# Kernel optimization log

Hardware: AMD Instinct MI355X
Metric: run time of the kernel (lower is better)

Reference implementation:

```python
import jax, jax.numpy as jnp
import numpy as np

N = 6000          # RPN proposals pre-NMS
C = 64            # ROI feature channels
NUM_CLASSES = 21  # VOC-style classes
THR = 0.7         # NMS IoU threshold (generate_rois default)


def setup_inputs() -> dict:
    key = jax.random.key(0)
    k = jax.random.split(key, 8)
    # valid boxes: x1<x2, y1<y2 inside a 1000x1000 image
    xy = jax.random.uniform(k[0], (N, 2)) * 900.0
    wh = jax.random.uniform(k[1], (N, 2)) * 90.0 + 10.0
    boxes = jnp.concatenate([xy, xy + wh], axis=-1)
    scores = jax.random.uniform(k[2], (N,))
    roi_features = jax.random.normal(k[3], (N, 14, 14, C))
    W1 = jax.random.normal(k[4], (2 * 2 * C, 1024)) * 0.02
    b1 = jnp.zeros((1024,))
    Wc = jax.random.normal(k[5], (1024, NUM_CLASSES)) * 0.02
    bc = jnp.zeros((NUM_CLASSES,))
    Wr = jax.random.normal(k[6], (1024, 4)) * 0.02
    br = jnp.zeros((4,))
    return dict(boxes=boxes, scores=scores, roi_features=roi_features,
                W1=W1, b1=b1, Wc=Wc, bc=bc, Wr=Wr, br=br)


def _nms_keep(boxes, scores, thr):
    # Greedy sequential NMS, identical math to the Python loop:
    # highest score kept, suppress any remaining box with IoU >= thr.
    order = jnp.argsort(-scores)
    b = boxes[order]
    x1, y1, x2, y2 = b[:, 0], b[:, 1], b[:, 2], b[:, 3]
    area = (x2 - x1) * (y2 - y1)
    ix1 = jnp.maximum(x1[:, None], x1[None, :])
    iy1 = jnp.maximum(y1[:, None], y1[None, :])
    ix2 = jnp.minimum(x2[:, None], x2[None, :])
    iy2 = jnp.minimum(y2[:, None], y2[None, :])
    inter = jnp.maximum(0.0, ix2 - ix1) * jnp.maximum(0.0, iy2 - iy1)  # [N,N]
    iou = inter / (area[:, None] + area[None, :] - inter)
    n = b.shape[0]
    idx = jnp.arange(n)

    def body(i, keep):
        # if box i survived, suppress later boxes with IoU >= thr
        sup = (iou[i] >= thr) & (idx > i) & keep[i]
        return keep & ~sup

    keep_sorted = jax.lax.fori_loop(0, n, body, jnp.ones(n, dtype=bool))
    return jnp.zeros(n, dtype=bool).at[order].set(keep_sorted)


def reference(boxes, scores, roi_features, W1, b1, Wc, bc, Wr, br):
    keep = _nms_keep(boxes, scores, THR)  # [N] bool, NMS-selected ROIs
    n = roi_features.shape[0]
    # MaxPooling2D(pool_size=7, stride=7): 14x14 -> 2x2
    pooled = roi_features.reshape(n, 2, 7, 2, 7, C).max(axis=(2, 4))
    flat = pooled.reshape(n, -1)                      # [N, 256]
    h = jax.nn.relu(flat @ W1 + b1)                   # [N, 1024]
    cls = jax.nn.softmax(h @ Wc + bc, axis=-1)        # [N, num_classes]
    reg = h @ Wr + br                                 # [N, 4]
    kf = keep.astype(cls.dtype)[:, None]
    # suppressed ROIs zeroed (static-shape stand-in for the variable-length selection)
    return cls * kf, reg * kf, keep
```

## Files before the change

kernel.cpp:

```cpp
#include <hip/hip_runtime.h>

using u64 = unsigned long long;
using u32 = unsigned int;
using u16 = unsigned short;

typedef short bf16x8 __attribute__((ext_vector_type(8)));
typedef float f32x4  __attribute__((ext_vector_type(4)));

#define NB   6000
#define CB94 94
#define THRF 0.7f

__device__ __forceinline__ u16 f2bf(float f) {
    u32 u = __float_as_uint(f);
    return (u16)((u + 0x7FFFu + ((u >> 16) & 1u)) >> 16);
}

__device__ __forceinline__ void gload_lds16(const void* g, void* l) {
    __builtin_amdgcn_global_load_lds((const __attribute__((address_space(1))) void*)g,
                                     (__attribute__((address_space(3))) void*)l, 16, 0, 0);
}


__global__ void rank_kernel(const float* __restrict__ scores, int* __restrict__ rank) {
    __shared__ float sj[256];
    int t = threadIdx.x;
    int j0 = blockIdx.y * 256;
    int jj = j0 + t;
    sj[t] = (jj < NB) ? scores[jj] : 0.f;
    __syncthreads();
    int i = blockIdx.x * 256 + t;
    if (i >= NB) return;
    float si = scores[i];
    int jn = min(256, NB - j0);
    int cnt = 0;
    for (int k = 0; k < jn; ++k) {
        float s = sj[k];
        int j = j0 + k;
        cnt += (s > si) || (s == si && j < i);
    }
    if (cnt) atomicAdd(&rank[i], cnt);
}

__global__ void scatter_kernel(const float* __restrict__ boxes, const int* __restrict__ rank,
                               int* __restrict__ order, float4* __restrict__ sboxes) {
    int i = blockIdx.x * 256 + threadIdx.x;
    if (i >= NB) return;
    int r = rank[i];
    order[r] = i;
    sboxes[r] = ((const float4*)boxes)[i];
}

__global__ __launch_bounds__(64) void mask_kernel(const float4* __restrict__ sboxes,
                                                  u64* __restrict__ mask,
                                                  u64* __restrict__ bitmap) {
    int cb = blockIdx.x, rb = blockIdx.y;
    if (cb < rb) return;
    __shared__ float4 cbox[64];
    __shared__ float  carea[64];
    int t = threadIdx.x;
    int j = cb * 64 + t;
    if (j < NB) {
        float4 b = sboxes[j];
        cbox[t] = b;
        carea[t] = (b.z - b.x) * (b.w - b.y);
    }
    __syncthreads();
    int i = rb * 64 + t;
    if (i >= NB) return;
    float4 a = sboxes[i];
    float aarea = (a.z - a.x) * (a.w - a.y);
    int jn = min(64, NB - cb * 64);
    u64 bits = 0;
    for (int k = 0; k < jn; ++k) {
        int jg = cb * 64 + k;
        if (jg <= i) continue;
        float4 b = cbox[k];
        float iw = fmaxf(fminf(a.z, b.z) - fmaxf(a.x, b.x), 0.f);
        float ih = fmaxf(fminf(a.w, b.w) - fmaxf(a.y, b.y), 0.f);
        float inter = __fmul_rn(iw, ih);
        float denom = __fsub_rn(__fadd_rn(aarea, carea[k]), inter);
        float iou = __fdiv_rn(inter, denom);
        if (iou >= THRF) bits |= 1ull << k;
    }
    mask[(size_t)i * CB94 + cb] = bits;
    if (bits) atomicOr(&bitmap[i * 2 + (cb >> 6)], 1ull << (cb & 63));
}

__global__ __launch_bounds__(256) void scan_kernel(const u64* __restrict__ gmask,
                                                   const u64* __restrict__ gbitmap,
                                                   const int* __restrict__ order,
                                                   float* __restrict__ keepF,
                                                   float* __restrict__ out) {
    __shared__ u64 diagLDS[CB94 * 64];
    __shared__ u64 bmLDS[NB * 2];
    __shared__ u64 removedLDS[CB94];
    int t = threadIdx.x;
    for (int idx = t; idx < CB94 * 64; idx += 256) {
        int w = idx >> 6, b = idx & 63;
        int r = w * 64 + b;
        diagLDS[idx] = (r < NB) ? gmask[(size_t)r * CB94 + w] : 0ull;
    }
    for (int idx = t; idx < NB * 2; idx += 256) bmLDS[idx] = gbitmap[idx];
    for (int idx = t; idx < CB94; idx += 256) removedLDS[idx] = 0ull;
    __syncthreads();

    if (t < 64) {
        int l = t;
        for (int w = 0; w < CB94; ++w) {
            u64 rm = removedLDS[w];
            u64 dg = diagLDS[w * 64 + l];
            u64 valid = (w == CB94 - 1) ? ((1ull << 48) - 1ull) : ~0ull;
            u64 nz = __ballot(dg != 0ull);
            u64 cand = nz & ~rm & valid;
            while (cand) {
                int b = __ffsll(cand) - 1;
                u64 db = __shfl(dg, b, 64);
                rm |= db;
                cand &= ~rm;
                cand &= ~(1ull << b);
            }
            if (l == 0) removedLDS[w] = rm;
            u64 kept = valid & ~rm;
            if ((kept >> l) & 1ull) {
                int r = w * 64 + l;
                u64 bm0 = bmLDS[2 * r], bm1 = bmLDS[2 * r + 1];
                if (w < 63) bm0 &= ~((2ull << w) - 1ull); else bm0 = 0ull;
                if (w >= 64) bm1 &= ~((2ull << (w - 64)) - 1ull);
                while (bm0) {
                    int tt = __ffsll(bm0) - 1;
                    bm0 &= bm0 - 1;
                    u64 mw = gmask[(size_t)r * CB94 + tt];
                    atomicOr(&removedLDS[tt], mw);
                }
                while (bm1) {
                    int b2 = __ffsll(bm1) - 1;
                    bm1 &= bm1 - 1;
                    int tt = 64 + b2;
                    u64 mw = gmask[(size_t)r * CB94 + tt];
                    atomicOr(&removedLDS[tt], mw);
                }
            }
        }
    }
    __syncthreads();
    for (int k = t; k < NB; k += 256) {
        int sup = (int)((removedLDS[k >> 6] >> (k & 63)) & 1ull);
        float kf = sup ? 0.f : 1.f;
        int orig = order[k];
        keepF[orig] = kf;
        out[150000 + orig] = kf;
    }
}


__global__ __launch_bounds__(256) void pool_kernel(const float* __restrict__ roi,
                                                   u16* __restrict__ flat) {
    int t = threadIdx.x;
    int n = blockIdx.x * 4 + (t >> 6);
    int lane = t & 63;
    int p = lane >> 4, li = lane & 15;
    int ph = p >> 1, pw = p & 1;
    const float4* base = (const float4*)roi;
    float mx0 = -3.4e38f, mx1 = -3.4e38f, mx2 = -3.4e38f, mx3 = -3.4e38f;
#pragma unroll
    for (int i = 0; i < 7; ++i)
#pragma unroll
        for (int j = 0; j < 7; ++j) {
            float4 v = base[((n * 14 + ph * 7 + i) * 14 + pw * 7 + j) * 16 + li];
            mx0 = fmaxf(mx0, v.x); mx1 = fmaxf(mx1, v.y);
            mx2 = fmaxf(mx2, v.z); mx3 = fmaxf(mx3, v.w);
        }
    int ob = n * 256 + p * 64 + li * 4;
    u64 pack = (u64)f2bf(mx0) | ((u64)f2bf(mx1) << 16) | ((u64)f2bf(mx2) << 32) | ((u64)f2bf(mx3) << 48);
    *(u64*)&flat[ob] = pack;
}

__global__ void prep_w1t(const float* __restrict__ W1, u16* __restrict__ w1t) {
    int idx = blockIdx.x * 256 + threadIdx.x;
    if (idx >= 1024 * 256) return;
    int n = idx >> 8, k = idx & 255;
    w1t[idx] = f2bf(W1[k * 1024 + n]);
}

__global__ void prep_w2t(const float* __restrict__ Wc, const float* __restrict__ Wr,
                         u16* __restrict__ w2t) {
    int idx = blockIdx.x * 256 + threadIdx.x;
    if (idx >= 32 * 1024) return;
    int o = idx >> 10, k = idx & 1023;
    float v = 0.f;
    if (o < 21) v = Wc[k * 21 + o];
    else if (o < 25) v = Wr[k * 4 + (o - 21)];
    w2t[idx] = f2bf(v);
}

__global__ __launch_bounds__(256) void gemm1_kernel(const u16* __restrict__ flat,
                                                    const u16* __restrict__ w1t,
                                                    const float* __restrict__ b1,
                                                    u16* __restrict__ h) {
    __shared__ __align__(16) u16 Alds[128 * 32];
    __shared__ __align__(16) u16 Blds[128 * 32];
    int t = threadIdx.x;
    int c0 = blockIdx.x * 128;
    int r0 = blockIdx.y * 128;
    int lane = t & 63, wid = t >> 6, wr = wid >> 1, wc = wid & 1;
    int lrow = lane & 15, kblk = lane >> 4;
    f32x4 acc[4][4] = {};
    for (int step = 0; step < 8; ++step) {
        int k0 = step * 32;
#pragma unroll
        for (int it = 0; it < 2; ++it) {
            int chunk = it * 256 + t;
            int row = chunk >> 2, kc = chunk & 3;
            int ar = r0 + row; ar = ar < (NB - 1) ? ar : (NB - 1);
            gload_lds16(flat + ar * 256 + k0 + kc * 8, &Alds[chunk * 8]);
            gload_lds16(w1t + (c0 + row) * 256 + k0 + kc * 8, &Blds[chunk * 8]);
        }
        __syncthreads();
        bf16x8 a[4], b[4];
#pragma unroll
        for (int m = 0; m < 4; ++m) a[m] = *(const bf16x8*)&Alds[(wr * 64 + m * 16 + lrow) * 32 + kblk * 8];
#pragma unroll
        for (int n = 0; n < 4; ++n) b[n] = *(const bf16x8*)&Blds[(wc * 64 + n * 16 + lrow) * 32 + kblk * 8];
#pragma unroll
        for (int m = 0; m < 4; ++m)
#pragma unroll
            for (int n = 0; n < 4; ++n)
                acc[m][n] = __builtin_amdgcn_mfma_f32_16x16x32_bf16(a[m], b[n], acc[m][n], 0, 0, 0);
        __syncthreads();
    }
    int rj = lane >> 4;
#pragma unroll
    for (int n = 0; n < 4; ++n) {
        int col = c0 + wc * 64 + n * 16 + lrow;
        float bias = b1[col];
#pragma unroll
        for (int m = 0; m < 4; ++m) {
            int rbase = r0 + wr * 64 + m * 16 + rj * 4;
#pragma unroll
            for (int j = 0; j < 4; ++j) {
                int r = rbase + j;
                if (r < NB) {
                    float v = acc[m][n][j] + bias;
                    v = v > 0.f ? v : 0.f;
                    h[r * 1024 + col] = f2bf(v);
                }
            }
        }
    }
}

__global__ __launch_bounds__(256) void gemm2_kernel(const u16* __restrict__ h,
                                                    const u16* __restrict__ w2t,
                                                    float* __restrict__ scores) {
    __shared__ __align__(16) u16 Alds[4 * 64 * 32];
    __shared__ __align__(16) u16 Blds[4 * 32 * 32];
    int t = threadIdx.x, lane = t & 63, w = t >> 6;
    int r0 = blockIdx.x * 64;
    int lrow = lane & 15, kblk = lane >> 4;
    f32x4 acc[2] = {};
    for (int round = 0; round < 8; ++round) {
        int kr0 = round * 128;
#pragma unroll
        for (int it = 0; it < 4; ++it) {
            int chunk = it * 256 + t;
            int kk = chunk >> 8, rem = chunk & 255, row = rem >> 2, kc = rem & 3;
            int ar = r0 + row; ar = ar < (NB - 1) ? ar : (NB - 1);
            gload_lds16(h + ar * 1024 + kr0 + kk * 32 + kc * 8, &Alds[chunk * 8]);
        }
#pragma unroll
        for (int it = 0; it < 2; ++it) {
            int chunk = it * 256 + t;
            int kk = chunk >> 7, rem = chunk & 127, orow = rem >> 2, kc = rem & 3;
            gload_lds16(w2t + orow * 1024 + kr0 + kk * 32 + kc * 8, &Blds[chunk * 8]);
        }
        __syncthreads();
#pragma unroll
        for (int kk = 0; kk < 4; ++kk) {
            bf16x8 a = *(const bf16x8*)&Alds[kk * 2048 + (w * 16 + lrow) * 32 + kblk * 8];
#pragma unroll
            for (int nf = 0; nf < 2; ++nf) {
                bf16x8 b = *(const bf16x8*)&Blds[kk * 1024 + (nf * 16 + lrow) * 32 + kblk * 8];
                acc[nf] = __builtin_amdgcn_mfma_f32_16x16x32_bf16(a, b, acc[nf], 0, 0, 0);
            }
        }
        __syncthreads();
    }
#pragma unroll
    for (int nf = 0; nf < 2; ++nf) {
        int col = nf * 16 + lrow;
#pragma unroll
        for (int j = 0; j < 4; ++j) {
            int r = r0 + w * 16 + (lane >> 4) * 4 + j;
            if (r < NB) scores[r * 32 + col] = acc[nf][j];
        }
    }
}

__global__ void epilogue_kernel(const float* __restrict__ scores, const float* __restrict__ keepF,
                                const float* __restrict__ bc, const float* __restrict__ br,
                                float* __restrict__ out) {
    int r = blockIdx.x * 256 + threadIdx.x;
    if (r >= NB) return;
    float kf = keepF[r];
    float lg[21];
    float m = -3.4e38f;
#pragma unroll
    for (int o = 0; o < 21; ++o) {
        lg[o] = scores[r * 32 + o] + bc[o];
        m = fmaxf(m, lg[o]);
    }
    float s = 0.f;
#pragma unroll
    for (int o = 0; o < 21; ++o) {
        lg[o] = expf(lg[o] - m);
        s += lg[o];
    }
    float inv = kf / s;
#pragma unroll
    for (int o = 0; o < 21; ++o) out[r * 21 + o] = lg[o] * inv;
#pragma unroll
    for (int o = 0; o < 4; ++o) out[126000 + r * 4 + o] = (scores[r * 32 + 21 + o] + br[o]) * kf;
}


extern "C" void kernel_launch(void* const* d_in, const int* in_sizes, int n_in,
                              void* d_out, int out_size, void* d_ws, size_t ws_size,
                              hipStream_t stream) {
    (void)in_sizes; (void)n_in; (void)out_size; (void)ws_size;
    const float* boxes  = (const float*)d_in[0];
    const float* scores = (const float*)d_in[1];
    const float* roi    = (const float*)d_in[2];
    const float* W1     = (const float*)d_in[3];
    const float* b1     = (const float*)d_in[4];
    const float* Wc     = (const float*)d_in[5];
    const float* bc     = (const float*)d_in[6];
    const float* Wr     = (const float*)d_in[7];
    const float* br     = (const float*)d_in[8];
    float* out = (float*)d_out;

    char* ws = (char*)d_ws;
    const size_t O_RANK   = 0;
    const size_t O_ORDER  = 24064;
    const size_t O_SBOX   = 48128;
    const size_t O_BITMAP = 144128;
    const size_t O_MASK   = 240128;
    const size_t O_KEEPF  = 4752128;
    const size_t O_FLAT   = 4776128;
    const size_t O_W1T    = 7848128;
    const size_t O_W2T    = 8372416;
    const size_t O_H      = 8437952;
    const size_t O_SCORES = 20725952;

    int*    rank   = (int*)(ws + O_RANK);
    int*    order  = (int*)(ws + O_ORDER);
    float4* sboxes = (float4*)(ws + O_SBOX);
    u64*    bitmap = (u64*)(ws + O_BITMAP);
    u64*    mask   = (u64*)(ws + O_MASK);
    float*  keepF  = (float*)(ws + O_KEEPF);
    u16*    flat   = (u16*)(ws + O_FLAT);
    u16*    w1t    = (u16*)(ws + O_W1T);
    u16*    w2t    = (u16*)(ws + O_W2T);
    u16*    h      = (u16*)(ws + O_H);
    float*  sc2    = (float*)(ws + O_SCORES);

    hipMemsetAsync(ws + O_RANK, 0, 24000, stream);
    hipMemsetAsync(ws + O_BITMAP, 0, 96000, stream);

    pool_kernel<<<1500, 256, 0, stream>>>(roi, flat);
    prep_w1t<<<1024, 256, 0, stream>>>(W1, w1t);
    prep_w2t<<<128, 256, 0, stream>>>(Wc, Wr, w2t);

    rank_kernel<<<dim3(24, 24), 256, 0, stream>>>(scores, rank);
    scatter_kernel<<<24, 256, 0, stream>>>(boxes, rank, order, sboxes);
    mask_kernel<<<dim3(CB94, CB94), 64, 0, stream>>>(sboxes, mask, bitmap);

    gemm1_kernel<<<dim3(8, 47), 256, 0, stream>>>(flat, w1t, b1, h);

    scan_kernel<<<1, 256, 0, stream>>>(mask, bitmap, order, keepF, out);

    gemm2_kernel<<<CB94, 256, 0, stream>>>(h, w2t, sc2);
    epilogue_kernel<<<24, 256, 0, stream>>>(sc2, keepF, bc, br, out);
}
```

Baseline: 220.9 us.

## Fuse front-end kernels, rank+scatter, contiguous diag mask, and gemm2 with epilogue

Merges pooling, weight transposes, and the score ranking with scatter into one heterogeneous front kernel. Rank is now computed per 64-row block without atomics, and the bitmap is cleared in place, which removes both memsets. The mask kernel now uses 256-thread blocks and also writes a contiguous diagonal array, so the single-block scan loads it with coalesced reads instead of strided ones. gemm2 is fused with the softmax/regression epilogue through LDS, removing a scores round-trip and a launch. The cost is a serial 6000-score loop per rank block, about 94 blocks, and some block-size imbalance within the fused front kernel.

```diff
diff --git a/kernel.cpp b/kernel.cpp
--- a/kernel.cpp
+++ b/kernel.cpp
@@ -22,51 +22,105 @@
 }
 
 
-__global__ void rank_kernel(const float* __restrict__ scores, int* __restrict__ rank) {
-    __shared__ float sj[256];
+__global__ __launch_bounds__(256) void front_kernel(
+        const float* __restrict__ roi, const float* __restrict__ W1,
+        const float* __restrict__ Wc, const float* __restrict__ Wr,
+        const float* __restrict__ scores, const float* __restrict__ boxes,
+        u16* __restrict__ flat, u16* __restrict__ w1t, u16* __restrict__ w2t,
+        int* __restrict__ order, float4* __restrict__ sboxes, u64* __restrict__ bitmap) {
+    __shared__ float sj[1024];
+    __shared__ int part[4][64];
+    int bid = blockIdx.x;
     int t = threadIdx.x;
-    int j0 = blockIdx.y * 256;
-    int jj = j0 + t;
-    sj[t] = (jj < NB) ? scores[jj] : 0.f;
-    __syncthreads();
-    int i = blockIdx.x * 256 + t;
-    if (i >= NB) return;
-    float si = scores[i];
-    int jn = min(256, NB - j0);
-    int cnt = 0;
-    for (int k = 0; k < jn; ++k) {
-        float s = sj[k];
-        int j = j0 + k;
-        cnt += (s > si) || (s == si && j < i);
-    }
-    if (cnt) atomicAdd(&rank[i], cnt);
-}
-
-__global__ void scatter_kernel(const float* __restrict__ boxes, const int* __restrict__ rank,
-                               int* __restrict__ order, float4* __restrict__ sboxes) {
-    int i = blockIdx.x * 256 + threadIdx.x;
-    if (i >= NB) return;
-    int r = rank[i];
-    order[r] = i;
-    sboxes[r] = ((const float4*)boxes)[i];
-}
-
-__global__ __launch_bounds__(64) void mask_kernel(const float4* __restrict__ sboxes,
-                                                  u64* __restrict__ mask,
-                                                  u64* __restrict__ bitmap) {
-    int cb = blockIdx.x, rb = blockIdx.y;
-    if (cb < rb) return;
+
+    if (bid < 1500) {
+        int n = bid * 4 + (t >> 6);
+        int lane = t & 63;
+        int p = lane >> 4, li = lane & 15;
+        int ph = p >> 1, pw = p & 1;
+        const float4* base = (const float4*)roi;
+        float mx0 = -3.4e38f, mx1 = -3.4e38f, mx2 = -3.4e38f, mx3 = -3.4e38f;
+#pragma unroll
+        for (int i = 0; i < 7; ++i)
+#pragma unroll
+            for (int j = 0; j < 7; ++j) {
+                float4 v = base[((n * 14 + ph * 7 + i) * 14 + pw * 7 + j) * 16 + li];
+                mx0 = fmaxf(mx0, v.x); mx1 = fmaxf(mx1, v.y);
+                mx2 = fmaxf(mx2, v.z); mx3 = fmaxf(mx3, v.w);
+            }
+        int ob = n * 256 + p * 64 + li * 4;
+        u64 pack = (u64)f2bf(mx0) | ((u64)f2bf(mx1) << 16) | ((u64)f2bf(mx2) << 32) | ((u64)f2bf(mx3) << 48);
+        *(u64*)&flat[ob] = pack;
+    } else if (bid < 2652) {
+        int idx = (bid - 1500) * 256 + t;
+        if (idx < 1024 * 256) {
+            int n = idx >> 8, k = idx & 255;
+            w1t[idx] = f2bf(W1[k * 1024 + n]);
+        } else {
+            int idx2 = idx - 1024 * 256;
+            if (idx2 < 32 * 1024) {
+                int o = idx2 >> 10, k = idx2 & 1023;
+                float v = 0.f;
+                if (o < 21) v = Wc[k * 21 + o];
+                else if (o < 25) v = Wr[k * 4 + (o - 21)];
+                w2t[idx2] = f2bf(v);
+            }
+        }
+    } else {
+        int rb = bid - 2652;
+        int li = t & 63;
+        int q = t >> 6;
+        int gi = rb * 64 + li;
+        float si = (gi < NB) ? scores[gi] : -1.f;
+        int cnt = 0;
+        for (int c0 = 0; c0 < NB; c0 += 1024) {
+#pragma unroll
+            for (int u = 0; u < 4; ++u) {
+                int jj = c0 + u * 256 + t;
+                sj[u * 256 + t] = (jj < NB) ? scores[jj] : -1e30f;
+            }
+            __syncthreads();
+            int lim = min(1024, NB - c0);
+            for (int k = q; k < lim; k += 4) {
+                float s = sj[k];
+                int j = c0 + k;
+                cnt += (s > si) || (s == si && j < gi);
+            }
+            __syncthreads();
+        }
+        part[q][li] = cnt;
+        __syncthreads();
+        if (t < 64 && gi < NB) {
+            int r = part[0][t] + part[1][t] + part[2][t] + part[3][t];
+            order[r] = gi;
+            sboxes[r] = ((const float4*)boxes)[gi];
+            bitmap[2 * r] = 0ull;
+            bitmap[2 * r + 1] = 0ull;
+        }
+    }
+}
+
+
+__global__ __launch_bounds__(256) void mask_kernel(const float4* __restrict__ sboxes,
+                                                   u64* __restrict__ mask,
+                                                   u64* __restrict__ diag,
+                                                   u64* __restrict__ bitmap) {
+    int cb = blockIdx.x;
+    int r0 = blockIdx.y * 256;
+    if (cb * 64 + 63 <= r0) return;
     __shared__ float4 cbox[64];
     __shared__ float  carea[64];
     int t = threadIdx.x;
-    int j = cb * 64 + t;
-    if (j < NB) {
-        float4 b = sboxes[j];
-        cbox[t] = b;
-        carea[t] = (b.z - b.x) * (b.w - b.y);
+    if (t < 64) {
+        int j = cb * 64 + t;
+        if (j < NB) {
+            float4 b = sboxes[j];
+            cbox[t] = b;
+            carea[t] = (b.z - b.x) * (b.w - b.y);
+        }
     }
     __syncthreads();
-    int i = rb * 64 + t;
+    int i = r0 + t;
     if (i >= NB) return;
     float4 a = sboxes[i];
     float aarea = (a.z - a.x) * (a.w - a.y);
@@ -84,10 +138,13 @@
         if (iou >= THRF) bits |= 1ull << k;
     }
     mask[(size_t)i * CB94 + cb] = bits;
+    if (cb == (i >> 6)) diag[i] = bits;
     if (bits) atomicOr(&bitmap[i * 2 + (cb >> 6)], 1ull << (cb & 63));
 }
 
+
 __global__ __launch_bounds__(256) void scan_kernel(const u64* __restrict__ gmask,
+                                                   const u64* __restrict__ gdiag,
                                                    const u64* __restrict__ gbitmap,
                                                    const int* __restrict__ order,
                                                    float* __restrict__ keepF,
@@ -96,11 +153,8 @@
     __shared__ u64 bmLDS[NB * 2];
     __shared__ u64 removedLDS[CB94];
     int t = threadIdx.x;
-    for (int idx = t; idx < CB94 * 64; idx += 256) {
-        int w = idx >> 6, b = idx & 63;
-        int r = w * 64 + b;
-        diagLDS[idx] = (r < NB) ? gmask[(size_t)r * CB94 + w] : 0ull;
-    }
+    for (int idx = t; idx < CB94 * 64; idx += 256)
+        diagLDS[idx] = (idx < NB) ? gdiag[idx] : 0ull;
     for (int idx = t; idx < NB * 2; idx += 256) bmLDS[idx] = gbitmap[idx];
     for (int idx = t; idx < CB94; idx += 256) removedLDS[idx] = 0ull;
     __syncthreads();
@@ -154,46 +208,6 @@
 }
 
 
-__global__ __launch_bounds__(256) void pool_kernel(const float* __restrict__ roi,
-                                                   u16* __restrict__ flat) {
-    int t = threadIdx.x;
-    int n = blockIdx.x * 4 + (t >> 6);
-    int lane = t & 63;
-    int p = lane >> 4, li = lane & 15;
-    int ph = p >> 1, pw = p & 1;
-    const float4* base = (const float4*)roi;
-    float mx0 = -3.4e38f, mx1 = -3.4e38f, mx2 = -3.4e38f, mx3 = -3.4e38f;
-#pragma unroll
-    for (int i = 0; i < 7; ++i)
-#pragma unroll
-        for (int j = 0; j < 7; ++j) {
-            float4 v = base[((n * 14 + ph * 7 + i) * 14 + pw * 7 + j) * 16 + li];
-            mx0 = fmaxf(mx0, v.x); mx1 = fmaxf(mx1, v.y);
-            mx2 = fmaxf(mx2, v.z); mx3 = fmaxf(mx3, v.w);
-        }
-    int ob = n * 256 + p * 64 + li * 4;
-    u64 pack = (u64)f2bf(mx0) | ((u64)f2bf(mx1) << 16) | ((u64)f2bf(mx2) << 32) | ((u64)f2bf(mx3) << 48);
-    *(u64*)&flat[ob] = pack;
-}
-
-__global__ void prep_w1t(const float* __restrict__ W1, u16* __restrict__ w1t) {
-    int idx = blockIdx.x * 256 + threadIdx.x;
-    if (idx >= 1024 * 256) return;
-    int n = idx >> 8, k = idx & 255;
-    w1t[idx] = f2bf(W1[k * 1024 + n]);
-}
-
-__global__ void prep_w2t(const float* __restrict__ Wc, const float* __restrict__ Wr,
-                         u16* __restrict__ w2t) {
-    int idx = blockIdx.x * 256 + threadIdx.x;
-    if (idx >= 32 * 1024) return;
-    int o = idx >> 10, k = idx & 1023;
-    float v = 0.f;
-    if (o < 21) v = Wc[k * 21 + o];
-    else if (o < 25) v = Wr[k * 4 + (o - 21)];
-    w2t[idx] = f2bf(v);
-}
-
 __global__ __launch_bounds__(256) void gemm1_kernel(const u16* __restrict__ flat,
                                                     const u16* __restrict__ w1t,
                                                     const float* __restrict__ b1,
@@ -250,11 +264,16 @@
     }
 }
 
-__global__ __launch_bounds__(256) void gemm2_kernel(const u16* __restrict__ h,
-                                                    const u16* __restrict__ w2t,
-                                                    float* __restrict__ scores) {
+
+__global__ __launch_bounds__(256) void gemm2epi_kernel(const u16* __restrict__ h,
+                                                       const u16* __restrict__ w2t,
+                                                       const float* __restrict__ keepF,
+                                                       const float* __restrict__ bc,
+                                                       const float* __restrict__ br,
+                                                       float* __restrict__ out) {
     __shared__ __align__(16) u16 Alds[4 * 64 * 32];
     __shared__ __align__(16) u16 Blds[4 * 32 * 32];
+    __shared__ float sc[64][33];
     int t = threadIdx.x, lane = t & 63, w = t >> 6;
     int r0 = blockIdx.x * 64;
     int lrow = lane & 15, kblk = lane >> 4;
@@ -291,36 +310,35 @@
         int col = nf * 16 + lrow;
 #pragma unroll
         for (int j = 0; j < 4; ++j) {
-            int r = r0 + w * 16 + (lane >> 4) * 4 + j;
-            if (r < NB) scores[r * 32 + col] = acc[nf][j];
-        }
-    }
-}
-
-__global__ void epilogue_kernel(const float* __restrict__ scores, const float* __restrict__ keepF,
-                                const float* __restrict__ bc, const float* __restrict__ br,
-                                float* __restrict__ out) {
-    int r = blockIdx.x * 256 + threadIdx.x;
-    if (r >= NB) return;
-    float kf = keepF[r];
-    float lg[21];
-    float m = -3.4e38f;
-#pragma unroll
-    for (int o = 0; o < 21; ++o) {
-        lg[o] = scores[r * 32 + o] + bc[o];
-        m = fmaxf(m, lg[o]);
-    }
-    float s = 0.f;
-#pragma unroll
-    for (int o = 0; o < 21; ++o) {
-        lg[o] = expf(lg[o] - m);
-        s += lg[o];
-    }
-    float inv = kf / s;
-#pragma unroll
-    for (int o = 0; o < 21; ++o) out[r * 21 + o] = lg[o] * inv;
-#pragma unroll
-    for (int o = 0; o < 4; ++o) out[126000 + r * 4 + o] = (scores[r * 32 + 21 + o] + br[o]) * kf;
+            int lr = w * 16 + (lane >> 4) * 4 + j;
+            sc[lr][col] = acc[nf][j];
+        }
+    }
+    __syncthreads();
+    if (t < 64) {
+        int r = r0 + t;
+        if (r < NB) {
+            float kf = keepF[r];
+            float lg[21];
+            float m = -3.4e38f;
+#pragma unroll
+            for (int o = 0; o < 21; ++o) {
+                lg[o] = sc[t][o] + bc[o];
+                m = fmaxf(m, lg[o]);
+            }
+            float s = 0.f;
+#pragma unroll
+            for (int o = 0; o < 21; ++o) {
+                lg[o] = expf(lg[o] - m);
+                s += lg[o];
+            }
+            float inv = kf / s;
+#pragma unroll
+            for (int o = 0; o < 21; ++o) out[r * 21 + o] = lg[o] * inv;
+#pragma unroll
+            for (int o = 0; o < 4; ++o) out[126000 + r * 4 + o] = (sc[t][21 + o] + br[o]) * kf;
+        }
+    }
 }
 
 
@@ -340,45 +358,32 @@
     float* out = (float*)d_out;
 
     char* ws = (char*)d_ws;
-    const size_t O_RANK   = 0;
-    const size_t O_ORDER  = 24064;
-    const size_t O_SBOX   = 48128;
-    const size_t O_BITMAP = 144128;
-    const size_t O_MASK   = 240128;
-    const size_t O_KEEPF  = 4752128;
-    const size_t O_FLAT   = 4776128;
-    const size_t O_W1T    = 7848128;
-    const size_t O_W2T    = 8372416;
-    const size_t O_H      = 8437952;
-    const size_t O_SCORES = 20725952;
-
-    int*    rank   = (int*)(ws + O_RANK);
+    const size_t O_ORDER  = 0;
+    const size_t O_SBOX   = 24064;
+    const size_t O_BITMAP = 120064;
+    const size_t O_DIAG   = 216064;
+    const size_t O_MASK   = 264192;
+    const size_t O_KEEPF  = 4776192;
+    const size_t O_FLAT   = 4800256;
+    const size_t O_W1T    = 7872256;
+    const size_t O_W2T    = 8396544;
+    const size_t O_H      = 8462080;
+
     int*    order  = (int*)(ws + O_ORDER);
     float4* sboxes = (float4*)(ws + O_SBOX);
     u64*    bitmap = (u64*)(ws + O_BITMAP);
+    u64*    diag   = (u64*)(ws + O_DIAG);
     u64*    mask   = (u64*)(ws + O_MASK);
     float*  keepF  = (float*)(ws + O_KEEPF);
     u16*    flat   = (u16*)(ws + O_FLAT);
     u16*    w1t    = (u16*)(ws + O_W1T);
     u16*    w2t    = (u16*)(ws + O_W2T);
     u16*    h      = (u16*)(ws + O_H);
-    float*  sc2    = (float*)(ws + O_SCORES);
-
-    hipMemsetAsync(ws + O_RANK, 0, 24000, stream);
-    hipMemsetAsync(ws + O_BITMAP, 0, 96000, stream);
-
-    pool_kernel<<<1500, 256, 0, stream>>>(roi, flat);
-    prep_w1t<<<1024, 256, 0, stream>>>(W1, w1t);
-    prep_w2t<<<128, 256, 0, stream>>>(Wc, Wr, w2t);
-
-    rank_kernel<<<dim3(24, 24), 256, 0, stream>>>(scores, rank);
-    scatter_kernel<<<24, 256, 0, stream>>>(boxes, rank, order, sboxes);
-    mask_kernel<<<dim3(CB94, CB94), 64, 0, stream>>>(sboxes, mask, bitmap);
-
+
+    front_kernel<<<2746, 256, 0, stream>>>(roi, W1, Wc, Wr, scores, boxes,
+                                           flat, w1t, w2t, order, sboxes, bitmap);
+    mask_kernel<<<dim3(CB94, 24), 256, 0, stream>>>(sboxes, mask, diag, bitmap);
+    scan_kernel<<<1, 256, 0, stream>>>(mask, diag, bitmap, order, keepF, out);
     gemm1_kernel<<<dim3(8, 47), 256, 0, stream>>>(flat, w1t, b1, h);
-
-    scan_kernel<<<1, 256, 0, stream>>>(mask, bitmap, order, keepF, out);
-
-    gemm2_kernel<<<CB94, 256, 0, stream>>>(h, w2t, sc2);
-    epilogue_kernel<<<24, 256, 0, stream>>>(sc2, keepF, bc, br, out);
-}
+    gemm2epi_kernel<<<CB94, 256, 0, stream>>>(h, w2t, keepF, bc, br, out);
+}
```

After: 232.2 us. 1.05x slower.
